# Kernel optimization log

Measured on AMD Instinct MI355X. Metric: run time of the kernel, lower is better.

Reference implementation:

```python
import jax, jax.numpy as jnp
import numpy as np

B, N1, N2, C1, C2, MLP_OUT = 16, 4096, 1024, 128, 256, 256


def setup_inputs() -> dict:
    key = jax.random.key(0)
    k = jax.random.split(key, 8)
    xyz1 = jax.random.normal(k[0], (B, N1, 3), dtype=jnp.float32)
    feat1 = jax.random.normal(k[1], (B, N1, C1), dtype=jnp.float32)
    xyz2 = jax.random.normal(k[2], (B, N2, 3), dtype=jnp.float32)
    feat2 = jax.random.normal(k[3], (B, N2, C2), dtype=jnp.float32)
    d_in = C1 + C2
    W1 = jax.random.normal(k[4], (d_in, MLP_OUT), dtype=jnp.float32) / np.sqrt(d_in)
    b1 = jnp.zeros((MLP_OUT,), dtype=jnp.float32)
    W2 = jax.random.normal(k[5], (MLP_OUT, MLP_OUT), dtype=jnp.float32) / np.sqrt(MLP_OUT)
    b2 = jnp.zeros((MLP_OUT,), dtype=jnp.float32)
    return {"xyz1": xyz1, "feat1": feat1, "xyz2": xyz2, "feat2": feat2,
            "W1": W1, "b1": b1, "W2": W2, "b2": b2}


def reference(xyz1, feat1, xyz2, feat2, W1, b1, W2, b2):
    # squared pairwise distances [B, N1, N2]
    dists = jnp.sum((xyz1[:, :, None, :] - xyz2[:, None, :, :]) ** 2, axis=-1)
    # 3 nearest neighbors (smallest distances)
    neg_d3, idx = jax.lax.top_k(-dists, 3)      # [B, N1, 3]
    d3 = jnp.maximum(-neg_d3, 1e-10)
    w = 1.0 / d3
    w = w / jnp.sum(w, axis=-1, keepdims=True)   # [B, N1, 3]
    # gather neighbor features: [B, N1, 3, C2]
    neighbor_feats = jax.vmap(lambda f, i: f[i])(feat2, idx)
    interpolated = jnp.sum(w[..., None] * neighbor_feats, axis=2)  # [B, N1, C2]
    new_feat = jnp.concatenate([interpolated, feat1], axis=-1)     # [B, N1, C2+C1]
    h = jax.nn.relu(new_feat @ W1 + b1)
    return jax.nn.relu(h @ W2 + b2)
```

## Files before the change

kernel.cpp:

```cpp
#include <hip/hip_runtime.h>
#include <cstdint>
#include <cstddef>

typedef unsigned short ushort_t;
typedef unsigned int uint_t;

typedef __bf16 bf16x8 __attribute__((ext_vector_type(8)));
typedef float floatx4 __attribute__((ext_vector_type(4)));

#define B_ 16
#define N1_ 4096
#define N2_ 1024
#define C1_ 128
#define C2_ 256
#define DIN_ 384
#define DOUT_ 256
#define M_ (B_ * N1_)

#define ASTRIDE 392
#define HSTRIDE 264


__device__ __forceinline__ ushort_t f2bf(float f) {
  unsigned int u = __builtin_bit_cast(unsigned int, f);
  u = (u + 0x7fffu + ((u >> 16) & 1u)) >> 16;
  return (ushort_t)u;
}


__global__ __launch_bounds__(256) void prep_kernel(
    const float* __restrict__ W1, const float* __restrict__ W2,
    ushort_t* __restrict__ W1s, ushort_t* __restrict__ W2s) {
  int e = blockIdx.x * 256 + threadIdx.x;
  if (e < DOUT_ * DIN_) {
    int kk = e & 31, n = (e >> 5) & 255, t = e >> 13;
    W1s[e] = f2bf(W1[(size_t)(t * 32 + kk) * DOUT_ + n]);
  }
  if (e < DOUT_ * DOUT_) {
    int kk = e & 31, n = (e >> 5) & 255, t = e >> 13;
    W2s[e] = f2bf(W2[(size_t)(t * 32 + kk) * DOUT_ + n]);
  }
}


__device__ __forceinline__ void ins_exact(float& s0, float& s1, float& s2,
                                          int& i0, int& i1, int& i2,
                                          float d, int p) {
  float ns2 = __builtin_amdgcn_fmed3f(d, s1, s2);
  float ns1 = __builtin_amdgcn_fmed3f(d, s0, s1);
  float ns0 = fminf(d, s0);
  bool c0 = d < s0, c1 = d < s1, c2 = d < s2;
  i2 = c1 ? i1 : (c2 ? p : i2);
  i1 = c0 ? i0 : (c1 ? p : i1);
  i0 = c0 ? p : i0;
  s0 = ns0; s1 = ns1; s2 = ns2;
}

__device__ __forceinline__ void ins_merge(float& s0, float& s1, float& s2,
                                          int& i0, int& i1, int& i2,
                                          float e, int j) {
  bool t0 = (e < s0) || (e == s0 && j < i0);
  bool t1 = (e < s1) || (e == s1 && j < i1);
  bool t2 = (e < s2) || (e == s2 && j < i2);
  s2 = t1 ? s1 : (t2 ? e : s2);
  i2 = t1 ? i1 : (t2 ? j : i2);
  s1 = t0 ? s0 : (t1 ? e : s1);
  i1 = t0 ? i0 : (t1 ? j : i1);
  s0 = t0 ? e : s0;
  i0 = t0 ? j : i0;
}

__global__ __launch_bounds__(256) void knn_kernel(
    const float* __restrict__ xyz1, const float* __restrict__ xyz2,
    int* __restrict__ idx_out, float* __restrict__ w_out) {
  __shared__ float4 xs4[N2_];
  int b = blockIdx.x >> 7;
  int n1base = (blockIdx.x & 127) << 5;
  const float* p2 = xyz2 + (size_t)b * N2_ * 3;
  for (int i = threadIdx.x; i < N2_; i += 256) {
    const float* s = p2 + 3 * i;
    xs4[i] = make_float4(s[0], s[1], s[2], 0.0f);
  }
  __syncthreads();

  int g = threadIdx.x >> 3;
  int sub = threadIdx.x & 7;
  int row = b * N1_ + n1base + g;
  const float* p1 = xyz1 + (size_t)row * 3;
  float x1 = p1[0], y1 = p1[1], z1 = p1[2];

  float s0 = 3.0e38f, s1 = 3.0e38f, s2 = 3.0e38f;
  int i0 = 0, i1 = 0, i2 = 0;

  int p = sub;
#pragma unroll 8
  for (int t = 0; t < N2_ / 8; ++t) {
    float4 qv = xs4[p];
    float dx = x1 - qv.x;
    float dy = y1 - qv.y;
    float dz = z1 - qv.z;
    float d = dx * dx + dy * dy + dz * dz;
    ins_exact(s0, s1, s2, i0, i1, i2, d, p);
    p += 8;
  }

#pragma unroll
  for (int mm = 1; mm <= 4; mm <<= 1) {
    float e0 = __shfl_xor(s0, mm), e1 = __shfl_xor(s1, mm), e2 = __shfl_xor(s2, mm);
    int j0 = __shfl_xor(i0, mm), j1 = __shfl_xor(i1, mm), j2 = __shfl_xor(i2, mm);
    ins_merge(s0, s1, s2, i0, i1, i2, e0, j0);
    ins_merge(s0, s1, s2, i0, i1, i2, e1, j1);
    ins_merge(s0, s1, s2, i0, i1, i2, e2, j2);
  }

  if (sub == 0) {
    float r0 = 1.0f / fmaxf(s0, 1e-10f);
    float r1 = 1.0f / fmaxf(s1, 1e-10f);
    float r2 = 1.0f / fmaxf(s2, 1e-10f);
    float s = 1.0f / (r0 + r1 + r2);
    int base = row * 3;
    idx_out[base + 0] = i0;
    idx_out[base + 1] = i1;
    idx_out[base + 2] = i2;
    w_out[base + 0] = r0 * s;
    w_out[base + 1] = r1 * s;
    w_out[base + 2] = r2 * s;
  }
}


__global__ __launch_bounds__(256, 3) void fused_kernel(
    const float* __restrict__ feat1, const float* __restrict__ feat2,
    const int* __restrict__ idx, const float* __restrict__ w,
    const ushort_t* __restrict__ W1s, const float* __restrict__ b1,
    const ushort_t* __restrict__ W2s, const float* __restrict__ b2,
    float* __restrict__ out) {
  __shared__ ushort_t As[64 * ASTRIDE];
  const int tid = threadIdx.x;
  const int wave = tid >> 6;
  const int lane = tid & 63;
  const int m = lane & 15;
  const int q = lane >> 4;
  const int rb = (blockIdx.x & 7) * 128 + (blockIdx.x >> 3);
  const int row0 = rb * 64;
  const int b = row0 >> 12;

  const int b_off = (wave * 64 + m) * 32 + q * 8;

  bf16x8 bf0[4], bf1[4];
#pragma unroll
  for (int j = 0; j < 4; ++j) bf0[j] = *(const bf16x8*)(W1s + b_off + j * 512);

#pragma unroll 8
  for (int it = 0; it < 16; ++it) {
    int rl = wave * 16 + it;
    int row = row0 + rl;
    const int* ip = idx + (size_t)row * 3;
    const float* wp = w + (size_t)row * 3;
    int i0 = ip[0], i1 = ip[1], i2 = ip[2];
    float w0 = wp[0], w1 = wp[1], w2 = wp[2];

    const float4* f0 = (const float4*)(feat2 + ((size_t)b * N2_ + i0) * C2_);
    const float4* f1 = (const float4*)(feat2 + ((size_t)b * N2_ + i1) * C2_);
    const float4* f2 = (const float4*)(feat2 + ((size_t)b * N2_ + i2) * C2_);
    float4 a = f0[lane];
    float4 c = f1[lane];
    float4 d = f2[lane];
    float vx = w0 * a.x + w1 * c.x + w2 * d.x;
    float vy = w0 * a.y + w1 * c.y + w2 * d.y;
    float vz = w0 * a.z + w1 * c.z + w2 * d.z;
    float vw = w0 * a.w + w1 * c.w + w2 * d.w;
    uint_t lo = (uint_t)f2bf(vx) | ((uint_t)f2bf(vy) << 16);
    uint_t hi = (uint_t)f2bf(vz) | ((uint_t)f2bf(vw) << 16);
    *(uint2*)&As[rl * ASTRIDE + 4 * lane] = make_uint2(lo, hi);

    float2 t1 = ((const float2*)(feat1 + (size_t)row * C1_))[lane];
    uint_t pk = (uint_t)f2bf(t1.x) | ((uint_t)f2bf(t1.y) << 16);
    *(uint_t*)&As[rl * ASTRIDE + 256 + 2 * lane] = pk;
  }
  __syncthreads();

  floatx4 acc[4][4];
#pragma unroll
  for (int i = 0; i < 4; ++i)
#pragma unroll
    for (int j = 0; j < 4; ++j) acc[i][j] = (floatx4)0.0f;

  {
    bf16x8 af[4];
#pragma unroll
    for (int t = 0; t < 12; t += 2) {
#pragma unroll
      for (int j = 0; j < 4; ++j)
        bf1[j] = *(const bf16x8*)(W1s + (size_t)(t + 1) * 8192 + b_off + j * 512);
#pragma unroll
      for (int i = 0; i < 4; ++i)
        af[i] = *(const bf16x8*)&As[(m + 16 * i) * ASTRIDE + t * 32 + q * 8];
#pragma unroll
      for (int i = 0; i < 4; ++i)
#pragma unroll
        for (int j = 0; j < 4; ++j)
          acc[i][j] = __builtin_amdgcn_mfma_f32_16x16x32_bf16(af[i], bf0[j],
                                                              acc[i][j], 0, 0, 0);
      if (t + 2 < 12) {
#pragma unroll
        for (int j = 0; j < 4; ++j)
          bf0[j] = *(const bf16x8*)(W1s + (size_t)(t + 2) * 8192 + b_off + j * 512);
      }
#pragma unroll
      for (int i = 0; i < 4; ++i)
        af[i] = *(const bf16x8*)&As[(m + 16 * i) * ASTRIDE + (t + 1) * 32 + q * 8];
#pragma unroll
      for (int i = 0; i < 4; ++i)
#pragma unroll
        for (int j = 0; j < 4; ++j)
          acc[i][j] = __builtin_amdgcn_mfma_f32_16x16x32_bf16(af[i], bf1[j],
                                                              acc[i][j], 0, 0, 0);
    }
  }

#pragma unroll
  for (int j = 0; j < 4; ++j) bf0[j] = *(const bf16x8*)(W2s + b_off + j * 512);

  __syncthreads();

  ushort_t* HS = As;
#pragma unroll
  for (int j = 0; j < 4; ++j) {
    int col = wave * 64 + j * 16 + m;
    float bv = b1[col];
#pragma unroll
    for (int i = 0; i < 4; ++i)
#pragma unroll
      for (int r = 0; r < 4; ++r) {
        int row = i * 16 + q * 4 + r;
        float v = acc[i][j][r] + bv;
        v = v > 0.0f ? v : 0.0f;
        HS[row * HSTRIDE + col] = f2bf(v);
      }
  }
  __syncthreads();

  floatx4 acc2[4][4];
#pragma unroll
  for (int i = 0; i < 4; ++i)
#pragma unroll
    for (int j = 0; j < 4; ++j) acc2[i][j] = (floatx4)0.0f;

  {
    bf16x8 af[4];
#pragma unroll
    for (int t = 0; t < 8; t += 2) {
#pragma unroll
      for (int j = 0; j < 4; ++j)
        bf1[j] = *(const bf16x8*)(W2s + (size_t)(t + 1) * 8192 + b_off + j * 512);
#pragma unroll
      for (int i = 0; i < 4; ++i)
        af[i] = *(const bf16x8*)&HS[(m + 16 * i) * HSTRIDE + t * 32 + q * 8];
#pragma unroll
      for (int i = 0; i < 4; ++i)
#pragma unroll
        for (int j = 0; j < 4; ++j)
          acc2[i][j] = __builtin_amdgcn_mfma_f32_16x16x32_bf16(af[i], bf0[j],
                                                               acc2[i][j], 0, 0, 0);
      if (t + 2 < 8) {
#pragma unroll
        for (int j = 0; j < 4; ++j)
          bf0[j] = *(const bf16x8*)(W2s + (size_t)(t + 2) * 8192 + b_off + j * 512);
      }
#pragma unroll
      for (int i = 0; i < 4; ++i)
        af[i] = *(const bf16x8*)&HS[(m + 16 * i) * HSTRIDE + (t + 1) * 32 + q * 8];
#pragma unroll
      for (int i = 0; i < 4; ++i)
#pragma unroll
        for (int j = 0; j < 4; ++j)
          acc2[i][j] = __builtin_amdgcn_mfma_f32_16x16x32_bf16(af[i], bf1[j],
                                                               acc2[i][j], 0, 0, 0);
    }
  }

#pragma unroll
  for (int j = 0; j < 4; ++j) {
    int col = wave * 64 + j * 16 + m;
    float bv = b2[col];
#pragma unroll
    for (int i = 0; i < 4; ++i)
#pragma unroll
      for (int r = 0; r < 4; ++r) {
        int row = i * 16 + q * 4 + r;
        float v = acc2[i][j][r] + bv;
        v = v > 0.0f ? v : 0.0f;
        out[(size_t)(row0 + row) * DOUT_ + col] = v;
      }
  }
}


constexpr size_t OFF_W1S = 0;
constexpr size_t OFF_W2S = OFF_W1S + 196608;
constexpr size_t OFF_IDX = OFF_W2S + 131072;
constexpr size_t OFF_W = OFF_IDX + 786432;
constexpr size_t WS_TOTAL = OFF_W + 786432;

extern "C" void kernel_launch(void* const* d_in, const int* in_sizes, int n_in,
                              void* d_out, int out_size, void* d_ws, size_t ws_size,
                              hipStream_t stream) {
  const float* xyz1 = (const float*)d_in[0];
  const float* feat1 = (const float*)d_in[1];
  const float* xyz2 = (const float*)d_in[2];
  const float* feat2 = (const float*)d_in[3];
  const float* W1 = (const float*)d_in[4];
  const float* b1 = (const float*)d_in[5];
  const float* W2 = (const float*)d_in[6];
  const float* b2 = (const float*)d_in[7];

  if (ws_size < WS_TOTAL) return;

  char* ws = (char*)d_ws;
  ushort_t* W1s = (ushort_t*)(ws + OFF_W1S);
  ushort_t* W2s = (ushort_t*)(ws + OFF_W2S);
  int* idx = (int*)(ws + OFF_IDX);
  float* w = (float*)(ws + OFF_W);

  prep_kernel<<<384, 256, 0, stream>>>(W1, W2, W1s, W2s);
  knn_kernel<<<B_ * (N1_ / 32), 256, 0, stream>>>(xyz1, xyz2, idx, w);
  fused_kernel<<<M_ / 64, 256, 0, stream>>>(feat1, feat2, idx, w, W1s, b1, W2s,
                                            b2, (float*)d_out);
}
```

Measured before the change: 193.4 us.

## Fuse kNN search into the fused MLP kernel, keep neighbors in shared memory

Removes the separate kNN kernel and computes the 3-nearest-neighbor search at the start of each fused block. The xyz2 points are staged in the As shared buffer and indices and weights go to small shared arrays, so the idx/w global round trip and one launch are gone. Each block now handles 64 query rows with 4 threads per row instead of 8, which gives a longer serial scan per thread. The kNN phase also runs at the fused kernel's occupancy (launch bounds 3), and the MFMA work cannot start until the scan finishes.

```diff
diff --git a/kernel.cpp b/kernel.cpp
--- a/kernel.cpp
+++ b/kernel.cpp
@@ -26,22 +26,6 @@
   u = (u + 0x7fffu + ((u >> 16) & 1u)) >> 16;
   return (ushort_t)u;
 }
-
-
-__global__ __launch_bounds__(256) void prep_kernel(
-    const float* __restrict__ W1, const float* __restrict__ W2,
-    ushort_t* __restrict__ W1s, ushort_t* __restrict__ W2s) {
-  int e = blockIdx.x * 256 + threadIdx.x;
-  if (e < DOUT_ * DIN_) {
-    int kk = e & 31, n = (e >> 5) & 255, t = e >> 13;
-    W1s[e] = f2bf(W1[(size_t)(t * 32 + kk) * DOUT_ + n]);
-  }
-  if (e < DOUT_ * DOUT_) {
-    int kk = e & 31, n = (e >> 5) & 255, t = e >> 13;
-    W2s[e] = f2bf(W2[(size_t)(t * 32 + kk) * DOUT_ + n]);
-  }
-}
-
 
 __device__ __forceinline__ void ins_exact(float& s0, float& s1, float& s2,
                                           int& i0, int& i1, int& i2,
@@ -70,72 +54,31 @@
   i0 = t0 ? j : i0;
 }
 
-__global__ __launch_bounds__(256) void knn_kernel(
+
+__global__ __launch_bounds__(256) void prep_kernel(
+    const float* __restrict__ W1, const float* __restrict__ W2,
+    ushort_t* __restrict__ W1s, ushort_t* __restrict__ W2s) {
+  int e = blockIdx.x * 256 + threadIdx.x;
+  if (e < DOUT_ * DIN_) {
+    int kk = e & 31, n = (e >> 5) & 255, t = e >> 13;
+    W1s[e] = f2bf(W1[(size_t)(t * 32 + kk) * DOUT_ + n]);
+  }
+  if (e < DOUT_ * DOUT_) {
+    int kk = e & 31, n = (e >> 5) & 255, t = e >> 13;
+    W2s[e] = f2bf(W2[(size_t)(t * 32 + kk) * DOUT_ + n]);
+  }
+}
+
+
+__global__ __launch_bounds__(256, 3) void fused_kernel(
     const float* __restrict__ xyz1, const float* __restrict__ xyz2,
-    int* __restrict__ idx_out, float* __restrict__ w_out) {
-  __shared__ float4 xs4[N2_];
-  int b = blockIdx.x >> 7;
-  int n1base = (blockIdx.x & 127) << 5;
-  const float* p2 = xyz2 + (size_t)b * N2_ * 3;
-  for (int i = threadIdx.x; i < N2_; i += 256) {
-    const float* s = p2 + 3 * i;
-    xs4[i] = make_float4(s[0], s[1], s[2], 0.0f);
-  }
-  __syncthreads();
-
-  int g = threadIdx.x >> 3;
-  int sub = threadIdx.x & 7;
-  int row = b * N1_ + n1base + g;
-  const float* p1 = xyz1 + (size_t)row * 3;
-  float x1 = p1[0], y1 = p1[1], z1 = p1[2];
-
-  float s0 = 3.0e38f, s1 = 3.0e38f, s2 = 3.0e38f;
-  int i0 = 0, i1 = 0, i2 = 0;
-
-  int p = sub;
-#pragma unroll 8
-  for (int t = 0; t < N2_ / 8; ++t) {
-    float4 qv = xs4[p];
-    float dx = x1 - qv.x;
-    float dy = y1 - qv.y;
-    float dz = z1 - qv.z;
-    float d = dx * dx + dy * dy + dz * dz;
-    ins_exact(s0, s1, s2, i0, i1, i2, d, p);
-    p += 8;
-  }
-
-#pragma unroll
-  for (int mm = 1; mm <= 4; mm <<= 1) {
-    float e0 = __shfl_xor(s0, mm), e1 = __shfl_xor(s1, mm), e2 = __shfl_xor(s2, mm);
-    int j0 = __shfl_xor(i0, mm), j1 = __shfl_xor(i1, mm), j2 = __shfl_xor(i2, mm);
-    ins_merge(s0, s1, s2, i0, i1, i2, e0, j0);
-    ins_merge(s0, s1, s2, i0, i1, i2, e1, j1);
-    ins_merge(s0, s1, s2, i0, i1, i2, e2, j2);
-  }
-
-  if (sub == 0) {
-    float r0 = 1.0f / fmaxf(s0, 1e-10f);
-    float r1 = 1.0f / fmaxf(s1, 1e-10f);
-    float r2 = 1.0f / fmaxf(s2, 1e-10f);
-    float s = 1.0f / (r0 + r1 + r2);
-    int base = row * 3;
-    idx_out[base + 0] = i0;
-    idx_out[base + 1] = i1;
-    idx_out[base + 2] = i2;
-    w_out[base + 0] = r0 * s;
-    w_out[base + 1] = r1 * s;
-    w_out[base + 2] = r2 * s;
-  }
-}
-
-
-__global__ __launch_bounds__(256, 3) void fused_kernel(
     const float* __restrict__ feat1, const float* __restrict__ feat2,
-    const int* __restrict__ idx, const float* __restrict__ w,
     const ushort_t* __restrict__ W1s, const float* __restrict__ b1,
     const ushort_t* __restrict__ W2s, const float* __restrict__ b2,
     float* __restrict__ out) {
   __shared__ ushort_t As[64 * ASTRIDE];
+  __shared__ int qidx[64][3];
+  __shared__ float qw[64][3];
   const int tid = threadIdx.x;
   const int wave = tid >> 6;
   const int lane = tid & 63;
@@ -145,6 +88,59 @@
   const int row0 = rb * 64;
   const int b = row0 >> 12;
 
+  float4* xs4 = (float4*)As;
+  const float* p2 = xyz2 + (size_t)b * N2_ * 3;
+  for (int i = tid; i < N2_; i += 256) {
+    const float* s = p2 + 3 * i;
+    xs4[i] = make_float4(s[0], s[1], s[2], 0.0f);
+  }
+  __syncthreads();
+
+  {
+    const int g = tid >> 2;
+    const int sub = tid & 3;
+    const float* p1 = xyz1 + (size_t)(row0 + g) * 3;
+    float x1 = p1[0], y1 = p1[1], z1 = p1[2];
+
+    float s0 = 3.0e38f, s1 = 3.0e38f, s2 = 3.0e38f;
+    int i0 = 0, i1 = 0, i2 = 0;
+
+    int p = sub;
+#pragma unroll 8
+    for (int t = 0; t < N2_ / 4; ++t) {
+      float4 qv = xs4[p];
+      float dx = x1 - qv.x;
+      float dy = y1 - qv.y;
+      float dz = z1 - qv.z;
+      float d = dx * dx + dy * dy + dz * dz;
+      ins_exact(s0, s1, s2, i0, i1, i2, d, p);
+      p += 4;
+    }
+
+#pragma unroll
+    for (int mm = 1; mm <= 2; mm <<= 1) {
+      float e0 = __shfl_xor(s0, mm), e1 = __shfl_xor(s1, mm), e2 = __shfl_xor(s2, mm);
+      int j0 = __shfl_xor(i0, mm), j1 = __shfl_xor(i1, mm), j2 = __shfl_xor(i2, mm);
+      ins_merge(s0, s1, s2, i0, i1, i2, e0, j0);
+      ins_merge(s0, s1, s2, i0, i1, i2, e1, j1);
+      ins_merge(s0, s1, s2, i0, i1, i2, e2, j2);
+    }
+
+    if (sub == 0) {
+      float r0 = 1.0f / fmaxf(s0, 1e-10f);
+      float r1 = 1.0f / fmaxf(s1, 1e-10f);
+      float r2 = 1.0f / fmaxf(s2, 1e-10f);
+      float s = 1.0f / (r0 + r1 + r2);
+      qidx[g][0] = i0;
+      qidx[g][1] = i1;
+      qidx[g][2] = i2;
+      qw[g][0] = r0 * s;
+      qw[g][1] = r1 * s;
+      qw[g][2] = r2 * s;
+    }
+  }
+  __syncthreads();
+
   const int b_off = (wave * 64 + m) * 32 + q * 8;
 
   bf16x8 bf0[4], bf1[4];
@@ -155,10 +151,8 @@
   for (int it = 0; it < 16; ++it) {
     int rl = wave * 16 + it;
     int row = row0 + rl;
-    const int* ip = idx + (size_t)row * 3;
-    const float* wp = w + (size_t)row * 3;
-    int i0 = ip[0], i1 = ip[1], i2 = ip[2];
-    float w0 = wp[0], w1 = wp[1], w2 = wp[2];
+    int i0 = qidx[rl][0], i1 = qidx[rl][1], i2 = qidx[rl][2];
+    float w0 = qw[rl][0], w1 = qw[rl][1], w2 = qw[rl][2];
 
     const float4* f0 = (const float4*)(feat2 + ((size_t)b * N2_ + i0) * C2_);
     const float4* f1 = (const float4*)(feat2 + ((size_t)b * N2_ + i1) * C2_);
@@ -299,9 +293,7 @@
 
 constexpr size_t OFF_W1S = 0;
 constexpr size_t OFF_W2S = OFF_W1S + 196608;
-constexpr size_t OFF_IDX = OFF_W2S + 131072;
-constexpr size_t OFF_W = OFF_IDX + 786432;
-constexpr size_t WS_TOTAL = OFF_W + 786432;
+constexpr size_t WS_TOTAL = OFF_W2S + 131072;
 
 extern "C" void kernel_launch(void* const* d_in, const int* in_sizes, int n_in,
                               void* d_out, int out_size, void* d_ws, size_t ws_size,
@@ -320,11 +312,8 @@
   char* ws = (char*)d_ws;
   ushort_t* W1s = (ushort_t*)(ws + OFF_W1S);
   ushort_t* W2s = (ushort_t*)(ws + OFF_W2S);
-  int* idx = (int*)(ws + OFF_IDX);
-  float* w = (float*)(ws + OFF_W);
 
   prep_kernel<<<384, 256, 0, stream>>>(W1, W2, W1s, W2s);
-  knn_kernel<<<B_ * (N1_ / 32), 256, 0, stream>>>(xyz1, xyz2, idx, w);
-  fused_kernel<<<M_ / 64, 256, 0, stream>>>(feat1, feat2, idx, w, W1s, b1, W2s,
-                                            b2, (float*)d_out);
-}
+  fused_kernel<<<M_ / 64, 256, 0, stream>>>(xyz1, xyz2, feat1, feat2, W1s, b1,
+                                            W2s, b2, (float*)d_out);
+}
```

Measured after the change: 209.9 us. 8.5% more time.
